# Performance work log

Measured on AMD Instinct MI355X. Metric: run time of the kernel, lower is better.

Reference implementation:

```python
import jax, jax.numpy as jnp
import numpy as np

B, N, C, K = 8, 4096, 128, 9
EPS = 1e-5


def setup_inputs() -> dict:
    key = jax.random.key(0)
    ks = jax.random.split(key, 8)
    x = jax.random.normal(ks[0], (B, N, C), jnp.float32)
    # fc1: Linear(C,C) + BN(C)
    W1 = jax.random.normal(ks[1], (C, C), jnp.float32) * 0.02
    b1 = jnp.zeros((C,), jnp.float32)
    g1 = jnp.ones((C,), jnp.float32)
    be1 = jnp.zeros((C,), jnp.float32)
    # graph conv MLP: Linear(2C,C) + BN(C) + GELU
    Wg = jax.random.normal(ks[2], (2 * C, C), jnp.float32) * 0.02
    bg = jnp.zeros((C,), jnp.float32)
    gg = jnp.ones((C,), jnp.float32)
    beg = jnp.zeros((C,), jnp.float32)
    # fc2: Linear(C,C) + BN(C)
    W2 = jax.random.normal(ks[3], (C, C), jnp.float32) * 0.02
    b2 = jnp.zeros((C,), jnp.float32)
    g2 = jnp.ones((C,), jnp.float32)
    be2 = jnp.zeros((C,), jnp.float32)
    return {"x": x, "W1": W1, "b1": b1, "g1": g1, "be1": be1,
            "Wg": Wg, "bg": bg, "gg": gg, "beg": beg,
            "W2": W2, "b2": b2, "g2": g2, "be2": be2}


def _bn(h, g, b):
    # BatchNorm1d in training mode: batch stats over the (B*N) axis, biased var
    m = jnp.mean(h, axis=0)
    v = jnp.var(h, axis=0)
    return g * (h - m) * jax.lax.rsqrt(v + EPS) + b


def reference(x, W1, b1, g1, be1, Wg, bg, gg, beg, W2, b2, g2, be2):
    Bd, Nd, Cd = x.shape
    residual = x
    # fc1
    h = _bn(x.reshape(Bd * Nd, Cd) @ W1 + b1, g1, be1).reshape(Bd, Nd, Cd)
    # KNN: pairwise squared distances, k smallest
    sq = jnp.sum(h * h, axis=-1, keepdims=True)              # [B,N,1]
    dist = sq - 2.0 * jnp.einsum('bnc,bmc->bnm', h, h) + sq.transpose(0, 2, 1)
    _, idx = jax.lax.top_k(-dist, K)                          # [B,N,K]
    # gather neighbors [B,N,K,C]
    nbrs = jax.vmap(lambda hb, ib: hb[ib])(h, idx)
    # max-relative aggregation
    agg = jnp.max(nbrs - h[:, :, None, :], axis=2)            # [B,N,C]
    cat = jnp.concatenate([h, agg], axis=-1).reshape(Bd * Nd, 2 * Cd)
    hg = jax.nn.gelu(_bn(cat @ Wg + bg, gg, beg), approximate=False)
    # fc2 + residual
    out = _bn(hg @ W2 + b2, g2, be2).reshape(Bd, Nd, Cd) + residual
    return out
```

## Files before the change

### kernel.cpp

```cpp
#include <hip/hip_runtime.h>
#include <hip/hip_bf16.h>
#include <float.h>
#include <math.h>

#define BB 8
#define NN 4096
#define CC 128
#define MROWS (BB * NN)
#define EPSBN 1e-5f

#define QB 64
#define CT 64
#define NTILE (NN / CT)

typedef __attribute__((ext_vector_type(8))) short bf16x8;
typedef __attribute__((ext_vector_type(4))) float f32x4;

#define GLOBAL_AS __attribute__((address_space(1)))
#define LDS_AS __attribute__((address_space(3)))

__device__ __forceinline__ ushort f2bf(float f) {
  uint u = __float_as_uint(f);
  u = u + 0x7fffu + ((u >> 16) & 1u);
  return (ushort)(u >> 16);
}
__device__ __forceinline__ float bf2f(ushort h) {
  return __uint_as_float(((uint)h) << 16);
}

#define GBM 64
#define GBN 128
#define GBK 32

__global__ __launch_bounds__(256)
void gemm_bias_kernel(const float* __restrict__ A, const float* __restrict__ W,
                      const float* __restrict__ bias, float* __restrict__ out,
                      int M, int K) {
  __shared__ float As[GBK][GBM + 4];
  __shared__ float Ws[GBK][GBN + 4];
  int tid = threadIdx.x;
  int m0 = blockIdx.x * GBM;
  int ty = tid >> 4, tx = tid & 15;

  float acc[4][8];
#pragma unroll
  for (int i = 0; i < 4; ++i)
#pragma unroll
    for (int j = 0; j < 8; ++j) acc[i][j] = 0.f;

  for (int k0 = 0; k0 < K; k0 += GBK) {
    {
      int row = tid >> 2, ch = tid & 3;
      const float* ap = A + (long)(m0 + row) * K + k0 + ch * 8;
      float4 a0 = *(const float4*)ap;
      float4 a1 = *(const float4*)(ap + 4);
      float av2[8] = {a0.x, a0.y, a0.z, a0.w, a1.x, a1.y, a1.z, a1.w};
#pragma unroll
      for (int e = 0; e < 8; ++e) As[ch * 8 + e][row] = av2[e];
    }
#pragma unroll
    for (int c = 0; c < 4; ++c) {
      int lin = tid + 256 * c;
      int row = lin >> 5, c4 = (lin & 31) * 4;
      *(float4*)&Ws[row][c4] = *(const float4*)&W[(long)(k0 + row) * GBN + c4];
    }
    __syncthreads();
#pragma unroll
    for (int kk = 0; kk < GBK; ++kk) {
      float4 a4 = *(const float4*)&As[kk][ty * 4];
      float4 b0 = *(const float4*)&Ws[kk][tx * 8];
      float4 b1 = *(const float4*)&Ws[kk][tx * 8 + 4];
      float av[4] = {a4.x, a4.y, a4.z, a4.w};
      float bv[8] = {b0.x, b0.y, b0.z, b0.w, b1.x, b1.y, b1.z, b1.w};
#pragma unroll
      for (int i = 0; i < 4; ++i)
#pragma unroll
        for (int j = 0; j < 8; ++j)
          acc[i][j] = fmaf(av[i], bv[j], acc[i][j]);
    }
    __syncthreads();
  }
  float4 bi0 = *(const float4*)&bias[tx * 8];
  float4 bi1 = *(const float4*)&bias[tx * 8 + 4];
#pragma unroll
  for (int i = 0; i < 4; ++i) {
    long r = (long)(m0 + ty * 4 + i);
    float4 o0 = {acc[i][0] + bi0.x, acc[i][1] + bi0.y, acc[i][2] + bi0.z, acc[i][3] + bi0.w};
    float4 o1 = {acc[i][4] + bi1.x, acc[i][5] + bi1.y, acc[i][6] + bi1.z, acc[i][7] + bi1.w};
    *(float4*)&out[r * GBN + tx * 8] = o0;
    *(float4*)&out[r * GBN + tx * 8 + 4] = o1;
  }
}

__global__ __launch_bounds__(256)
void colstats_kernel(const float* __restrict__ X, float* __restrict__ sum,
                     float* __restrict__ sumsq) {
  __shared__ float s1[256], s2[256];
  int tid = threadIdx.x;
  int c = tid & 127, rg = tid >> 7;
  int r0 = blockIdx.x * 256;
  float s = 0.f, ss = 0.f;
  for (int i = 0; i < 128; ++i) {
    float v = X[(long)(r0 + rg + i * 2) * CC + c];
    s += v; ss += v * v;
  }
  s1[tid] = s; s2[tid] = ss;
  __syncthreads();
  if (rg == 0) {
    s += s1[tid + 128]; ss += s2[tid + 128];
    atomicAdd(&sum[c], s);
    atomicAdd(&sumsq[c], ss);
  }
}

__global__ __launch_bounds__(256)
void bn_split_kernel(const float* __restrict__ X, const float* __restrict__ sum,
                     const float* __restrict__ sumsq, const float* __restrict__ g,
                     const float* __restrict__ be, float* __restrict__ cat,
                     ushort* __restrict__ hHi, ushort* __restrict__ hLo,
                     float* __restrict__ sqv) {
  int gid = blockIdx.x * 256 + threadIdx.x;
  int row = gid >> 5;
  int c4 = (gid & 31) * 4;
  const float inv = 1.0f / (float)MROWS;
  float4 x  = *(const float4*)&X[(long)row * CC + c4];
  float4 sm = *(const float4*)&sum[c4];
  float4 sq = *(const float4*)&sumsq[c4];
  float4 gv = *(const float4*)&g[c4];
  float4 bv = *(const float4*)&be[c4];
  float xv[4] = {x.x, x.y, x.z, x.w};
  float smv[4] = {sm.x, sm.y, sm.z, sm.w};
  float sqv2[4] = {sq.x, sq.y, sq.z, sq.w};
  float ga[4] = {gv.x, gv.y, gv.z, gv.w};
  float ba[4] = {bv.x, bv.y, bv.z, bv.w};
  float h[4];
  ushort hi[4], lo[4];
#pragma unroll
  for (int e = 0; e < 4; ++e) {
    float m = smv[e] * inv;
    float v = sqv2[e] * inv - m * m;
    float sc = ga[e] * rsqrtf(v + EPSBN);
    h[e] = (xv[e] - m) * sc + ba[e];
    hi[e] = f2bf(h[e]);
    lo[e] = f2bf(h[e] - bf2f(hi[e]));
  }
  float4 hv = {h[0], h[1], h[2], h[3]};
  *(float4*)&cat[(long)row * 256 + c4] = hv;
  ushort4 h4 = {hi[0], hi[1], hi[2], hi[3]};
  ushort4 l4 = {lo[0], lo[1], lo[2], lo[3]};
  *(ushort4*)&hHi[(long)row * CC + c4] = h4;
  *(ushort4*)&hLo[(long)row * CC + c4] = l4;
  float s = h[0] * h[0] + h[1] * h[1] + h[2] * h[2] + h[3] * h[3];
#pragma unroll
  for (int off = 16; off >= 1; off >>= 1) s += __shfl_xor(s, off, 64);
  if ((threadIdx.x & 31) == 0) sqv[row] = s;
}

__device__ __forceinline__ void insert9(float (&dk)[9], int (&ik)[9], float s, int idx) {
  bool sh[9];
#pragma unroll
  for (int k = 0; k < 9; ++k) sh[k] = s < dk[k];
#pragma unroll
  for (int k = 8; k >= 1; --k) {
    if (sh[k]) {
      bool up = sh[k - 1];
      dk[k] = up ? dk[k - 1] : s;
      ik[k] = up ? ik[k - 1] : idx;
    }
  }
  if (sh[0]) { dk[0] = s; ik[0] = idx; }
}

__device__ __forceinline__ void insert9_lex(float (&dk)[9], int (&ik)[9], float pd, int pi) {
  bool ins = (pd < dk[8]) || (pd == dk[8] && pi < ik[8]);
  if (ins) {
    bool sh[9];
#pragma unroll
    for (int t = 0; t < 9; ++t)
      sh[t] = (pd < dk[t]) || (pd == dk[t] && pi < ik[t]);
#pragma unroll
    for (int t = 8; t >= 1; --t) {
      if (sh[t]) {
        bool up = sh[t - 1];
        dk[t] = up ? dk[t - 1] : pd;
        ik[t] = up ? ik[t - 1] : pi;
      }
    }
    if (sh[0]) { dk[0] = pd; ik[0] = pi; }
  }
}

#define SCST 68

__global__ __attribute__((amdgpu_flat_work_group_size(256, 256), amdgpu_waves_per_eu(2, 2)))
void knn_agg_kernel(const ushort* __restrict__ hHi, const ushort* __restrict__ hLo,
                    const float* __restrict__ sqv, const float* __restrict__ cat,
                    float* __restrict__ catw) {
  __shared__ ushort csHi[CT * 128];
  __shared__ ushort csLo[CT * 128];
  __shared__ float  scoreT[CT * SCST];

  int tid = threadIdx.x;
  int wave = tid >> 6, lane = tid & 63;
  int l15 = lane & 15, quad = lane >> 4;
  int b = blockIdx.x & 7, qt = blockIdx.x >> 3;
  long brow = (long)b * NN;
  long rowbase = brow + (long)qt * QB;

  bf16x8 aHi[4][4], aLo[4][4];
#pragma unroll
  for (int rg = 0; rg < 4; ++rg) {
    long gq = rowbase + rg * 16 + l15;
    const ushort* ph = hHi + gq * CC + quad * 8;
    const ushort* pl = hLo + gq * CC + quad * 8;
#pragma unroll
    for (int ks = 0; ks < 4; ++ks) {
      aHi[rg][ks] = *(const bf16x8*)(ph + ks * 32);
      aLo[rg][ks] = *(const bf16x8*)(pl + ks * 32);
    }
  }

  float dk[9]; int ik[9];
#pragma unroll
  for (int k = 0; k < 9; ++k) { dk[k] = FLT_MAX; ik[k] = 0x7FFFFFFF; }
  int q = tid & 63, quarter = tid >> 6;

  {
    long gr = brow;
#pragma unroll
    for (int it = 0; it < 4; ++it) {
      int s0 = (wave * 4 + it) * 64;
      int s = s0 + lane;
      int r = s >> 4, dp = s & 15;
      int d = dp ^ (r & 7);
      const ushort* gH = hHi + (gr + r) * CC + d * 8;
      const ushort* gL = hLo + (gr + r) * CC + d * 8;
      __builtin_amdgcn_global_load_lds((const GLOBAL_AS void*)gH,
                                       (LDS_AS void*)&csHi[s0 * 8], 16, 0, 0);
      __builtin_amdgcn_global_load_lds((const GLOBAL_AS void*)gL,
                                       (LDS_AS void*)&csLo[s0 * 8], 16, 0, 0);
    }
  }
  __syncthreads();

#pragma unroll 1
  for (int ct = 0; ct < NTILE; ++ct) {
    int crow = wave * 16 + l15;
    float sqc = sqv[brow + (long)ct * CT + crow];
    f32x4 ac[4];
#pragma unroll
    for (int rg = 0; rg < 4; ++rg) { ac[rg].x = 0.f; ac[rg].y = 0.f; ac[rg].z = 0.f; ac[rg].w = 0.f; }
#pragma unroll
    for (int ks = 0; ks < 4; ++ks) {
      int sb = crow * 16 + ((ks * 4 + quad) ^ (crow & 7));
      bf16x8 bHi = *(const bf16x8*)&csHi[sb * 8];
      bf16x8 bLo = *(const bf16x8*)&csLo[sb * 8];
#pragma unroll
      for (int rg = 0; rg < 4; ++rg) {
        ac[rg] = __builtin_amdgcn_mfma_f32_16x16x32_bf16(aHi[rg][ks], bHi, ac[rg], 0, 0, 0);
        ac[rg] = __builtin_amdgcn_mfma_f32_16x16x32_bf16(aHi[rg][ks], bLo, ac[rg], 0, 0, 0);
        ac[rg] = __builtin_amdgcn_mfma_f32_16x16x32_bf16(aLo[rg][ks], bHi, ac[rg], 0, 0, 0);
      }
    }
#pragma unroll
    for (int rg = 0; rg < 4; ++rg) {
      float4 o = {fmaf(-2.f, ac[rg].x, sqc), fmaf(-2.f, ac[rg].y, sqc),
                  fmaf(-2.f, ac[rg].z, sqc), fmaf(-2.f, ac[rg].w, sqc)};
      *(float4*)&scoreT[crow * SCST + rg * 16 + quad * 4] = o;
    }
    __syncthreads();

    {
      int nt = (ct + 1) & (NTILE - 1);
      long gr = brow + (long)nt * CT;
#pragma unroll
      for (int it = 0; it < 4; ++it) {
        int s0 = (wave * 4 + it) * 64;
        int s = s0 + lane;
        int r = s >> 4, dp = s & 15;
        int d = dp ^ (r & 7);
        const ushort* gH = hHi + (gr + r) * CC + d * 8;
        const ushort* gL = hLo + (gr + r) * CC + d * 8;
        __builtin_amdgcn_global_load_lds((const GLOBAL_AS void*)gH,
                                         (LDS_AS void*)&csHi[s0 * 8], 16, 0, 0);
        __builtin_amdgcn_global_load_lds((const GLOBAL_AS void*)gL,
                                         (LDS_AS void*)&csLo[s0 * 8], 16, 0, 0);
      }
    }

    int gbase = ct * CT + quarter * 16;
    const float* scol = &scoreT[(quarter * 16) * SCST + q];
    float thr = dk[8];
#pragma unroll
    for (int jj = 0; jj < 16; jj += 4) {
      float s0 = scol[(jj + 0) * SCST];
      float s1 = scol[(jj + 1) * SCST];
      float s2 = scol[(jj + 2) * SCST];
      float s3 = scol[(jj + 3) * SCST];
      float mn = fminf(fminf(s0, s1), fminf(s2, s3));
      if (mn < thr) {
        if (s0 < thr) { insert9(dk, ik, s0, gbase + jj + 0); thr = dk[8]; }
        if (s1 < thr) { insert9(dk, ik, s1, gbase + jj + 1); thr = dk[8]; }
        if (s2 < thr) { insert9(dk, ik, s2, gbase + jj + 2); thr = dk[8]; }
        if (s3 < thr) { insert9(dk, ik, s3, gbase + jj + 3); thr = dk[8]; }
      }
    }
    __syncthreads();
  }

  float* mD = scoreT;
  int*   mI = (int*)(scoreT + 1728);
  int*   fI = (int*)(scoreT + 3456);
  if (quarter > 0) {
    int base = (quarter - 1) * 576 + q * 9;
#pragma unroll
    for (int k = 0; k < 9; ++k) { mD[base + k] = dk[k]; mI[base + k] = ik[k]; }
  }
  __syncthreads();
  if (quarter == 0) {
#pragma unroll 1
    for (int qq = 0; qq < 3; ++qq) {
      int base = qq * 576 + q * 9;
#pragma unroll 1
      for (int k = 0; k < 9; ++k)
        insert9_lex(dk, ik, mD[base + k], mI[base + k]);
    }
#pragma unroll
    for (int k = 0; k < 9; ++k) fI[q * 9 + k] = ik[k];
  }
  __syncthreads();

  int nb[9];
#pragma unroll
  for (int k = 0; k < 9; ++k) nb[k] = fI[q * 9 + k];
  long qrow = rowbase + q;
  const float4* cat4 = (const float4*)cat;
  float4* catw4 = (float4*)catw;
#pragma unroll 1
  for (int c4 = 0; c4 < 8; ++c4) {
    int cc = quarter * 8 + c4;
    float4 hq = cat4[qrow * 64 + cc];
    float4 mx = {-FLT_MAX, -FLT_MAX, -FLT_MAX, -FLT_MAX};
#pragma unroll
    for (int k = 0; k < 9; ++k) {
      float4 v = cat4[(brow + nb[k]) * 64 + cc];
      mx.x = fmaxf(mx.x, v.x - hq.x);
      mx.y = fmaxf(mx.y, v.y - hq.y);
      mx.z = fmaxf(mx.z, v.z - hq.z);
      mx.w = fmaxf(mx.w, v.w - hq.w);
    }
    catw4[qrow * 64 + 32 + cc] = mx;
  }
}

__global__ __launch_bounds__(256)
void bn_gelu_kernel(const float* __restrict__ X, const float* __restrict__ sum,
                    const float* __restrict__ sumsq, const float* __restrict__ g,
                    const float* __restrict__ be, float* __restrict__ out) {
  int gid = blockIdx.x * 256 + threadIdx.x;
  int row = gid >> 5;
  int c4 = (gid & 31) * 4;
  const float inv = 1.0f / (float)MROWS;
  float4 x  = *(const float4*)&X[(long)row * CC + c4];
  float4 sm = *(const float4*)&sum[c4];
  float4 sq = *(const float4*)&sumsq[c4];
  float4 gv = *(const float4*)&g[c4];
  float4 bv = *(const float4*)&be[c4];
  float xv[4] = {x.x, x.y, x.z, x.w};
  float smv[4] = {sm.x, sm.y, sm.z, sm.w};
  float sqv2[4] = {sq.x, sq.y, sq.z, sq.w};
  float ga[4] = {gv.x, gv.y, gv.z, gv.w};
  float ba[4] = {bv.x, bv.y, bv.z, bv.w};
  float o[4];
#pragma unroll
  for (int e = 0; e < 4; ++e) {
    float m = smv[e] * inv;
    float v = sqv2[e] * inv - m * m;
    float sc = ga[e] * rsqrtf(v + EPSBN);
    float h = (xv[e] - m) * sc + ba[e];
    o[e] = 0.5f * h * (1.0f + erff(h * 0.70710678118654752f));
  }
  float4 ov = {o[0], o[1], o[2], o[3]};
  *(float4*)&out[(long)row * CC + c4] = ov;
}

__global__ __launch_bounds__(256)
void bn_res_kernel(const float* __restrict__ X, const float* __restrict__ sum,
                   const float* __restrict__ sumsq, const float* __restrict__ g,
                   const float* __restrict__ be, const float* __restrict__ xres,
                   float* __restrict__ out) {
  int gid = blockIdx.x * 256 + threadIdx.x;
  int row = gid >> 5;
  int c4 = (gid & 31) * 4;
  const float inv = 1.0f / (float)MROWS;
  float4 x  = *(const float4*)&X[(long)row * CC + c4];
  float4 rr = *(const float4*)&xres[(long)row * CC + c4];
  float4 sm = *(const float4*)&sum[c4];
  float4 sq = *(const float4*)&sumsq[c4];
  float4 gv = *(const float4*)&g[c4];
  float4 bv = *(const float4*)&be[c4];
  float xv[4] = {x.x, x.y, x.z, x.w};
  float rv[4] = {rr.x, rr.y, rr.z, rr.w};
  float smv[4] = {sm.x, sm.y, sm.z, sm.w};
  float sqv2[4] = {sq.x, sq.y, sq.z, sq.w};
  float ga[4] = {gv.x, gv.y, gv.z, gv.w};
  float ba[4] = {bv.x, bv.y, bv.z, bv.w};
  float o[4];
#pragma unroll
  for (int e = 0; e < 4; ++e) {
    float m = smv[e] * inv;
    float v = sqv2[e] * inv - m * m;
    float sc = ga[e] * rsqrtf(v + EPSBN);
    o[e] = (xv[e] - m) * sc + ba[e] + rv[e];
  }
  float4 ov = {o[0], o[1], o[2], o[3]};
  *(float4*)&out[(long)row * CC + c4] = ov;
}

extern "C" void kernel_launch(void* const* d_in, const int* in_sizes, int n_in,
                              void* d_out, int out_size, void* d_ws, size_t ws_size,
                              hipStream_t stream) {
  const float* x   = (const float*)d_in[0];
  const float* W1  = (const float*)d_in[1];
  const float* b1  = (const float*)d_in[2];
  const float* g1  = (const float*)d_in[3];
  const float* be1 = (const float*)d_in[4];
  const float* Wg  = (const float*)d_in[5];
  const float* bg  = (const float*)d_in[6];
  const float* ggp = (const float*)d_in[7];
  const float* beg = (const float*)d_in[8];
  const float* W2  = (const float*)d_in[9];
  const float* b2  = (const float*)d_in[10];
  const float* g2  = (const float*)d_in[11];
  const float* be2 = (const float*)d_in[12];
  float* out = (float*)d_out;

  char* p = (char*)d_ws;
  auto alloc = [&](size_t bytes) {
    char* r = p;
    p += (bytes + 255) & ~(size_t)255;
    return r;
  };
  float*  bufA = (float*)alloc((size_t)MROWS * CC * 4);
  float*  cat  = (float*)alloc((size_t)MROWS * 256 * 4);
  ushort* hHi  = (ushort*)alloc((size_t)MROWS * CC * 2);
  ushort* hLo  = (ushort*)alloc((size_t)MROWS * CC * 2);
  float*  sqv  = (float*)alloc((size_t)MROWS * 4);
  float*  hg   = (float*)alloc((size_t)MROWS * CC * 4);
  float*  stats = (float*)alloc(6 * CC * 4);
  float* sum1 = stats,       *ss1 = stats + 128;
  float* sum2 = stats + 256, *ss2 = stats + 384;
  float* sum3 = stats + 512, *ss3 = stats + 640;

  hipMemsetAsync(stats, 0, 6 * CC * 4, stream);

  gemm_bias_kernel<<<MROWS / GBM, 256, 0, stream>>>(x, W1, b1, bufA, MROWS, CC);
  colstats_kernel<<<128, 256, 0, stream>>>(bufA, sum1, ss1);
  bn_split_kernel<<<MROWS / 8, 256, 0, stream>>>(bufA, sum1, ss1, g1, be1, cat, hHi, hLo, sqv);

  knn_agg_kernel<<<512, 256, 0, stream>>>(hHi, hLo, sqv, cat, cat);

  gemm_bias_kernel<<<MROWS / GBM, 256, 0, stream>>>(cat, Wg, bg, bufA, MROWS, 2 * CC);
  colstats_kernel<<<128, 256, 0, stream>>>(bufA, sum2, ss2);
  bn_gelu_kernel<<<MROWS / 8, 256, 0, stream>>>(bufA, sum2, ss2, ggp, beg, hg);

  gemm_bias_kernel<<<MROWS / GBM, 256, 0, stream>>>(hg, W2, b2, bufA, MROWS, CC);
  colstats_kernel<<<128, 256, 0, stream>>>(bufA, sum3, ss3);
  bn_res_kernel<<<MROWS / 8, 256, 0, stream>>>(bufA, sum3, ss3, g2, be2, x, out);
}
```

Before: 446.1 us.

## Fuse BN column stats into GEMM epilogue and retile KNN MFMA per wave

Removes the separate colstats kernels by accumulating per-column sum and sum of squares in the GEMM epilogue, first through LDS atomics and then global atomics. In the KNN kernel, each wave now computes a 32x32 block (two query groups by two candidate groups) instead of 64 queries by 16 candidates. This halves the A-fragment registers per wave, which may allow more overlap. It also precomputes the swizzled global source offsets so they are not recomputed every tile. The costs are more LDS B-fragment reads per wave and per-block shared-memory atomic contention in the GEMM epilogue.

Result: slower. 460.2 us (+3.2%).

```diff
diff --git a/kernel.cpp b/kernel.cpp
--- a/kernel.cpp
+++ b/kernel.cpp
@@ -33,14 +33,17 @@
 #define GBK 32
 
 __global__ __launch_bounds__(256)
-void gemm_bias_kernel(const float* __restrict__ A, const float* __restrict__ W,
-                      const float* __restrict__ bias, float* __restrict__ out,
-                      int M, int K) {
+void gemm_bias_stats_kernel(const float* __restrict__ A, const float* __restrict__ W,
+                            const float* __restrict__ bias, float* __restrict__ out,
+                            int M, int K, float* __restrict__ sum,
+                            float* __restrict__ sumsq) {
   __shared__ float As[GBK][GBM + 4];
   __shared__ float Ws[GBK][GBN + 4];
+  __shared__ float redS[GBN], redS2[GBN];
   int tid = threadIdx.x;
   int m0 = blockIdx.x * GBM;
   int ty = tid >> 4, tx = tid & 15;
+  if (tid < GBN) { redS[tid] = 0.f; redS2[tid] = 0.f; }
 
   float acc[4][8];
 #pragma unroll
@@ -80,36 +83,36 @@
     }
     __syncthreads();
   }
-  float4 bi0 = *(const float4*)&bias[tx * 8];
-  float4 bi1 = *(const float4*)&bias[tx * 8 + 4];
+  float bi[8];
+  *(float4*)&bi[0] = *(const float4*)&bias[tx * 8];
+  *(float4*)&bi[4] = *(const float4*)&bias[tx * 8 + 4];
+  float cs[8], css[8];
+#pragma unroll
+  for (int j = 0; j < 8; ++j) { cs[j] = 0.f; css[j] = 0.f; }
 #pragma unroll
   for (int i = 0; i < 4; ++i) {
     long r = (long)(m0 + ty * 4 + i);
-    float4 o0 = {acc[i][0] + bi0.x, acc[i][1] + bi0.y, acc[i][2] + bi0.z, acc[i][3] + bi0.w};
-    float4 o1 = {acc[i][4] + bi1.x, acc[i][5] + bi1.y, acc[i][6] + bi1.z, acc[i][7] + bi1.w};
+    float o[8];
+#pragma unroll
+    for (int j = 0; j < 8; ++j) {
+      o[j] = acc[i][j] + bi[j];
+      cs[j] += o[j];
+      css[j] += o[j] * o[j];
+    }
+    float4 o0 = {o[0], o[1], o[2], o[3]};
+    float4 o1 = {o[4], o[5], o[6], o[7]};
     *(float4*)&out[r * GBN + tx * 8] = o0;
     *(float4*)&out[r * GBN + tx * 8 + 4] = o1;
   }
-}
-
-__global__ __launch_bounds__(256)
-void colstats_kernel(const float* __restrict__ X, float* __restrict__ sum,
-                     float* __restrict__ sumsq) {
-  __shared__ float s1[256], s2[256];
-  int tid = threadIdx.x;
-  int c = tid & 127, rg = tid >> 7;
-  int r0 = blockIdx.x * 256;
-  float s = 0.f, ss = 0.f;
-  for (int i = 0; i < 128; ++i) {
-    float v = X[(long)(r0 + rg + i * 2) * CC + c];
-    s += v; ss += v * v;
-  }
-  s1[tid] = s; s2[tid] = ss;
+#pragma unroll
+  for (int j = 0; j < 8; ++j) {
+    atomicAdd(&redS[tx * 8 + j], cs[j]);
+    atomicAdd(&redS2[tx * 8 + j], css[j]);
+  }
   __syncthreads();
-  if (rg == 0) {
-    s += s1[tid + 128]; ss += s2[tid + 128];
-    atomicAdd(&sum[c], s);
-    atomicAdd(&sumsq[c], ss);
+  if (tid < GBN) {
+    atomicAdd(&sum[tid], redS[tid]);
+    atomicAdd(&sumsq[tid], redS2[tid]);
   }
 }
 
@@ -203,14 +206,15 @@
   int tid = threadIdx.x;
   int wave = tid >> 6, lane = tid & 63;
   int l15 = lane & 15, quad = lane >> 4;
+  int wq = wave >> 1, wc = wave & 1;
   int b = blockIdx.x & 7, qt = blockIdx.x >> 3;
   long brow = (long)b * NN;
   long rowbase = brow + (long)qt * QB;
 
-  bf16x8 aHi[4][4], aLo[4][4];
-#pragma unroll
-  for (int rg = 0; rg < 4; ++rg) {
-    long gq = rowbase + rg * 16 + l15;
+  bf16x8 aHi[2][4], aLo[2][4];
+#pragma unroll
+  for (int rg = 0; rg < 2; ++rg) {
+    long gq = rowbase + wq * 32 + rg * 16 + l15;
     const ushort* ph = hHi + gq * CC + quad * 8;
     const ushort* pl = hLo + gq * CC + quad * 8;
 #pragma unroll
@@ -220,24 +224,29 @@
     }
   }
 
+  int srcOff[4];
+#pragma unroll
+  for (int it = 0; it < 4; ++it) {
+    int s = (wave * 4 + it) * 64 + lane;
+    int r = s >> 4, dp = s & 15;
+    int d = dp ^ (r & 7);
+    srcOff[it] = r * CC + d * 8;
+  }
+
   float dk[9]; int ik[9];
 #pragma unroll
   for (int k = 0; k < 9; ++k) { dk[k] = FLT_MAX; ik[k] = 0x7FFFFFFF; }
   int q = tid & 63, quarter = tid >> 6;
 
   {
-    long gr = brow;
+    const ushort* baseH = hHi + brow * CC;
+    const ushort* baseL = hLo + brow * CC;
 #pragma unroll
     for (int it = 0; it < 4; ++it) {
       int s0 = (wave * 4 + it) * 64;
-      int s = s0 + lane;
-      int r = s >> 4, dp = s & 15;
-      int d = dp ^ (r & 7);
-      const ushort* gH = hHi + (gr + r) * CC + d * 8;
-      const ushort* gL = hLo + (gr + r) * CC + d * 8;
-      __builtin_amdgcn_global_load_lds((const GLOBAL_AS void*)gH,
+      __builtin_amdgcn_global_load_lds((const GLOBAL_AS void*)(baseH + srcOff[it]),
                                        (LDS_AS void*)&csHi[s0 * 8], 16, 0, 0);
-      __builtin_amdgcn_global_load_lds((const GLOBAL_AS void*)gL,
+      __builtin_amdgcn_global_load_lds((const GLOBAL_AS void*)(baseL + srcOff[it]),
                                        (LDS_AS void*)&csLo[s0 * 8], 16, 0, 0);
     }
   }
@@ -245,45 +254,56 @@
 
 #pragma unroll 1
   for (int ct = 0; ct < NTILE; ++ct) {
-    int crow = wave * 16 + l15;
-    float sqc = sqv[brow + (long)ct * CT + crow];
-    f32x4 ac[4];
-#pragma unroll
-    for (int rg = 0; rg < 4; ++rg) { ac[rg].x = 0.f; ac[rg].y = 0.f; ac[rg].z = 0.f; ac[rg].w = 0.f; }
+    float sqc[2];
+#pragma unroll
+    for (int cg = 0; cg < 2; ++cg)
+      sqc[cg] = sqv[brow + (long)ct * CT + wc * 32 + cg * 16 + l15];
+    f32x4 ac[2][2];
+#pragma unroll
+    for (int cg = 0; cg < 2; ++cg)
+#pragma unroll
+      for (int rg = 0; rg < 2; ++rg) { ac[cg][rg].x = 0.f; ac[cg][rg].y = 0.f; ac[cg][rg].z = 0.f; ac[cg][rg].w = 0.f; }
 #pragma unroll
     for (int ks = 0; ks < 4; ++ks) {
-      int sb = crow * 16 + ((ks * 4 + quad) ^ (crow & 7));
-      bf16x8 bHi = *(const bf16x8*)&csHi[sb * 8];
-      bf16x8 bLo = *(const bf16x8*)&csLo[sb * 8];
-#pragma unroll
-      for (int rg = 0; rg < 4; ++rg) {
-        ac[rg] = __builtin_amdgcn_mfma_f32_16x16x32_bf16(aHi[rg][ks], bHi, ac[rg], 0, 0, 0);
-        ac[rg] = __builtin_amdgcn_mfma_f32_16x16x32_bf16(aHi[rg][ks], bLo, ac[rg], 0, 0, 0);
-        ac[rg] = __builtin_amdgcn_mfma_f32_16x16x32_bf16(aLo[rg][ks], bHi, ac[rg], 0, 0, 0);
+      bf16x8 bHi[2], bLo[2];
+#pragma unroll
+      for (int cg = 0; cg < 2; ++cg) {
+        int crow = wc * 32 + cg * 16 + l15;
+        int sb = crow * 16 + ((ks * 4 + quad) ^ (crow & 7));
+        bHi[cg] = *(const bf16x8*)&csHi[sb * 8];
+        bLo[cg] = *(const bf16x8*)&csLo[sb * 8];
       }
-    }
-#pragma unroll
-    for (int rg = 0; rg < 4; ++rg) {
-      float4 o = {fmaf(-2.f, ac[rg].x, sqc), fmaf(-2.f, ac[rg].y, sqc),
-                  fmaf(-2.f, ac[rg].z, sqc), fmaf(-2.f, ac[rg].w, sqc)};
-      *(float4*)&scoreT[crow * SCST + rg * 16 + quad * 4] = o;
+#pragma unroll
+      for (int cg = 0; cg < 2; ++cg)
+#pragma unroll
+        for (int rg = 0; rg < 2; ++rg) {
+          ac[cg][rg] = __builtin_amdgcn_mfma_f32_16x16x32_bf16(aHi[rg][ks], bHi[cg], ac[cg][rg], 0, 0, 0);
+          ac[cg][rg] = __builtin_amdgcn_mfma_f32_16x16x32_bf16(aHi[rg][ks], bLo[cg], ac[cg][rg], 0, 0, 0);
+          ac[cg][rg] = __builtin_amdgcn_mfma_f32_16x16x32_bf16(aLo[rg][ks], bHi[cg], ac[cg][rg], 0, 0, 0);
+        }
+    }
+#pragma unroll
+    for (int cg = 0; cg < 2; ++cg) {
+      int crow = wc * 32 + cg * 16 + l15;
+#pragma unroll
+      for (int rg = 0; rg < 2; ++rg) {
+        float4 o = {fmaf(-2.f, ac[cg][rg].x, sqc[cg]), fmaf(-2.f, ac[cg][rg].y, sqc[cg]),
+                    fmaf(-2.f, ac[cg][rg].z, sqc[cg]), fmaf(-2.f, ac[cg][rg].w, sqc[cg])};
+        *(float4*)&scoreT[crow * SCST + wq * 32 + rg * 16 + quad * 4] = o;
+      }
     }
     __syncthreads();
 
     {
       int nt = (ct + 1) & (NTILE - 1);
-      long gr = brow + (long)nt * CT;
+      const ushort* baseH = hHi + (brow + (long)nt * CT) * CC;
+      const ushort* baseL = hLo + (brow + (long)nt * CT) * CC;
 #pragma unroll
       for (int it = 0; it < 4; ++it) {
         int s0 = (wave * 4 + it) * 64;
-        int s = s0 + lane;
-        int r = s >> 4, dp = s & 15;
-        int d = dp ^ (r & 7);
-        const ushort* gH = hHi + (gr + r) * CC + d * 8;
-        const ushort* gL = hLo + (gr + r) * CC + d * 8;
-        __builtin_amdgcn_global_load_lds((const GLOBAL_AS void*)gH,
+        __builtin_amdgcn_global_load_lds((const GLOBAL_AS void*)(baseH + srcOff[it]),
                                          (LDS_AS void*)&csHi[s0 * 8], 16, 0, 0);
-        __builtin_amdgcn_global_load_lds((const GLOBAL_AS void*)gL,
+        __builtin_amdgcn_global_load_lds((const GLOBAL_AS void*)(baseL + srcOff[it]),
                                          (LDS_AS void*)&csLo[s0 * 8], 16, 0, 0);
       }
     }
@@ -454,17 +474,14 @@
 
   hipMemsetAsync(stats, 0, 6 * CC * 4, stream);
 
-  gemm_bias_kernel<<<MROWS / GBM, 256, 0, stream>>>(x, W1, b1, bufA, MROWS, CC);
-  colstats_kernel<<<128, 256, 0, stream>>>(bufA, sum1, ss1);
+  gemm_bias_stats_kernel<<<MROWS / GBM, 256, 0, stream>>>(x, W1, b1, bufA, MROWS, CC, sum1, ss1);
   bn_split_kernel<<<MROWS / 8, 256, 0, stream>>>(bufA, sum1, ss1, g1, be1, cat, hHi, hLo, sqv);
 
   knn_agg_kernel<<<512, 256, 0, stream>>>(hHi, hLo, sqv, cat, cat);
 
-  gemm_bias_kernel<<<MROWS / GBM, 256, 0, stream>>>(cat, Wg, bg, bufA, MROWS, 2 * CC);
-  colstats_kernel<<<128, 256, 0, stream>>>(bufA, sum2, ss2);
+  gemm_bias_stats_kernel<<<MROWS / GBM, 256, 0, stream>>>(cat, Wg, bg, bufA, MROWS, 2 * CC, sum2, ss2);
   bn_gelu_kernel<<<MROWS / 8, 256, 0, stream>>>(bufA, sum2, ss2, ggp, beg, hg);
 
-  gemm_bias_kernel<<<MROWS / GBM, 256, 0, stream>>>(hg, W2, b2, bufA, MROWS, CC);
-  colstats_kernel<<<128, 256, 0, stream>>>(bufA, sum3, ss3);
+  gemm_bias_stats_kernel<<<MROWS / GBM, 256, 0, stream>>>(hg, W2, b2, bufA, MROWS, CC, sum3, ss3);
   bn_res_kernel<<<MROWS / 8, 256, 0, stream>>>(bufA, sum3, ss3, g2, be2, x, out);
 }
```
